# Kernel optimization log

Measured on AMD Instinct MI355X. Metric: run time of the kernel, lower is better.

Reference implementation:

```python
import jax, jax.numpy as jnp
import numpy as np


def _warp(x, flow):
    """Backward bilinear warp (grid_sample equivalent, zeros padding).

    x:    [B, C, H, W] feature frame
    flow: [B, 2, H, W] per-pixel motion vector (x, y) in pixels
    Samples x at (px + flow_x, py + flow_y) with bilinear interpolation;
    out-of-bounds samples contribute zero (padding_mode='zeros').
    """
    B, C, H, W = x.shape
    ys, xs = jnp.meshgrid(jnp.arange(H, dtype=x.dtype), jnp.arange(W, dtype=x.dtype), indexing='ij')
    gx = xs[None] + flow[:, 0]  # [B, H, W] sample x coords
    gy = ys[None] + flow[:, 1]  # [B, H, W] sample y coords
    x0 = jnp.floor(gx)
    y0 = jnp.floor(gy)
    wx = gx - x0
    wy = gy - y0
    flat = x.reshape(B, C, H * W)

    def corner(xi, yi, w):
        valid = (xi >= 0) & (xi <= W - 1) & (yi >= 0) & (yi <= H - 1)
        xc = jnp.clip(xi, 0, W - 1).astype(jnp.int32)
        yc = jnp.clip(yi, 0, H - 1).astype(jnp.int32)
        idx = (yc * W + xc).reshape(B, 1, H * W)
        v = jnp.take_along_axis(flat, idx, axis=2).reshape(B, C, H, W)
        return v * (w * valid.astype(x.dtype))[:, None]

    return (corner(x0, y0, (1.0 - wx) * (1.0 - wy))
            + corner(x0 + 1.0, y0, wx * (1.0 - wy))
            + corner(x0, y0 + 1.0, (1.0 - wx) * wy)
            + corner(x0 + 1.0, y0 + 1.0, wx * wy))


def setup_inputs() -> dict:
    key = jax.random.key(0)
    k1, k2 = jax.random.split(key)
    B, I, C, H, W = 2, 5, 16, 544, 960
    features = jax.random.normal(k1, (B, I, C, H, W), dtype=jnp.float32)
    mv = jax.random.normal(k2, (B, I, 2, H, W), dtype=jnp.float32) * 4.0  # ~4 px motion
    return {"features": features, "mv": mv}


def reference(features, mv):
    """Accumulative backward warp.

    Original torch loop: for i in 1..I-1: for j = i-1 .. 0:
        features[:, i] = warp(features[:, i], mv[:, j])
    i.e. frame i is sequentially warped by mv[i-1], mv[i-2], ..., mv[0].
    Equivalent vectorized form: for j = I-2 .. 0, warp all frames > j by
    mv[:, j] simultaneously (each frame still sees mv indices in descending
    order), removing the per-frame Python loop.
    """
    I = features.shape[1]
    warp_frames = jax.vmap(_warp, in_axes=(1, None), out_axes=1)  # over frame axis
    out = features
    for j in range(I - 2, -1, -1):
        warped = warp_frames(out[:, j + 1:], mv[:, j])  # [B, I-1-j, C, H, W]
        out = out.at[:, j + 1:].set(warped)
    return out
```

## Files before the change

### kernel.cpp

```cpp
#include <hip/hip_runtime.h>
#include <stdint.h>

namespace {
constexpr int Wd = 960, Hd = 544, Cd = 16, Id = 5, Bd = 2;
constexpr int HW = Hd * Wd;
constexpr long CHW = (long)Cd * HW;
constexpr long FRAME_BSTRIDE = (long)Id * CHW;
constexpr long FLOW_BSTRIDE  = (long)Id * 2 * HW;

constexpr int TSX = 64, TSY = 32;
constexpr int HALO = 12;
constexpr int TWX = TSX + 2 * HALO;
constexpr int TWY = TSY + 2 * HALO;
constexpr int NCHUNK = 20;
constexpr int TILE_F = NCHUNK * 256;
constexpr int GX = Wd / TSX;
constexpr int GY = Hd / TSY;
constexpr int NWG = GX * GY * Bd;
}

struct F2 { float x, y; };
struct Job {
  const void* s; long ss;
  void*       d; long ds;
  const float* fl;
  int sBF, dBF;
};

__device__ __forceinline__ uint f2bf_bits(float v) {
  uint x = __float_as_uint(v);
  return (x + 0x7FFFu + ((x >> 16) & 1u)) >> 16;
}

__global__ __launch_bounds__(512) void warp_jobs(
    Job j0, Job j1, Job j2, Job j3, Job j4)
{
  __shared__ float tile[2][TILE_F];

  const int jb = blockIdx.y;
  Job J = j0;
  if      (jb == 1) J = j1;
  else if (jb == 2) J = j2;
  else if (jb == 3) J = j3;
  else if (jb == 4) J = j4;

  const int orig = blockIdx.x;
  const int xcd  = orig & 7;
  constexpr int q = NWG / 8, r = NWG % 8;
  const int wgid = (xcd < r ? xcd * (q + 1) : r * (q + 1) + (xcd - r) * q)
                 + (orig >> 3);

  const int b   = wgid / (GX * GY);
  const int rem = wgid - b * (GX * GY);
  const int tyb = rem / GX;
  const int txb = rem - tyb * GX;
  const int X0 = txb * TSX;
  const int Y0 = tyb * TSY;

  const int t   = threadIdx.x;
  const int x   = X0 + ((t & 15) << 2);
  const int y   = Y0 + (t >> 4);
  const int pix = y * Wd + x;

  const float*    sF32 = (const float*)J.s + (long)b * J.ss;
  float*          dF32 = (float*)J.d + (long)b * J.ds;
  const uint16_t* sB16 = (const uint16_t*)J.s + (long)b * J.ss;
  uint16_t*       dB16 = (uint16_t*)J.d + (long)b * J.ds;
  const bool sBF = J.sBF != 0;
  const bool dBF = J.dBF != 0;

  if (J.fl == nullptr) {
#pragma unroll
    for (int c = 0; c < Cd; ++c)
      *reinterpret_cast<float4*>(dF32 + (long)c * HW + pix)
          = *reinterpret_cast<const float4*>(sF32 + (long)c * HW + pix);
    return;
  }

  const float* fl = J.fl + (long)b * FLOW_BSTRIDE;
  float4 fxv = *reinterpret_cast<const float4*>(fl + pix);
  float4 fyv = *reinterpret_cast<const float4*>(fl + HW + pix);

  float w00[4], w10[4], w01[4], w11[4];
  int   lA[4];
  int   g00[4], g10[4], g01[4], g11[4];

#pragma unroll
  for (int j = 0; j < 4; ++j) {
    float fx = (j == 0) ? fxv.x : (j == 1) ? fxv.y : (j == 2) ? fxv.z : fxv.w;
    float fy = (j == 0) ? fyv.x : (j == 1) ? fyv.y : (j == 2) ? fyv.z : fyv.w;
    float gx = (float)(x + j) + fx;
    float gy = (float)y + fy;
    float x0f = floorf(gx), y0f = floorf(gy);
    float wx = gx - x0f, wy = gy - y0f;
    bool vx0 = (x0f >= 0.f) && (x0f <= (float)(Wd - 1));
    bool vx1 = (x0f + 1.f >= 0.f) && (x0f + 1.f <= (float)(Wd - 1));
    bool vy0 = (y0f >= 0.f) && (y0f <= (float)(Hd - 1));
    bool vy1 = (y0f + 1.f >= 0.f) && (y0f + 1.f <= (float)(Hd - 1));
    w00[j] = (1.f - wx) * (1.f - wy) * ((vx0 && vy0) ? 1.f : 0.f);
    w10[j] = wx * (1.f - wy)         * ((vx1 && vy0) ? 1.f : 0.f);
    w01[j] = (1.f - wx) * wy         * ((vx0 && vy1) ? 1.f : 0.f);
    w11[j] = wx * wy                 * ((vx1 && vy1) ? 1.f : 0.f);
    int ix0 = (int)x0f;
    int iy0 = (int)y0f;
    int lx = ix0 - (X0 - HALO);
    int ly = iy0 - (Y0 - HALO);
    bool ft = (lx >= 0) & (lx <= TWX - 2) & (ly >= 0) & (ly <= TWY - 2);
    lA[j] = ft ? (ly * TWX + lx) * 4 : -1;
    int xc0 = min(max(ix0, 0), Wd - 1), xc1 = min(max(ix0 + 1, 0), Wd - 1);
    int yc0 = min(max(iy0, 0), Hd - 1), yc1 = min(max(iy0 + 1, 0), Hd - 1);
    g00[j] = yc0 * Wd + xc0;
    g10[j] = yc0 * Wd + xc1;
    g01[j] = yc1 * Wd + xc0;
    g11[j] = yc1 * Wd + xc1;
  }

  const int lane = t & 63;
  const int wv   = t >> 6;
  const int nck  = (wv < 4) ? 3 : 2;
  int goff[3];
#pragma unroll
  for (int k = 0; k < 3; ++k) {
    int ck = wv + 8 * k;
    if (ck < NCHUNK) {
      int foff = ck * 256 + lane * 4;
      int ly = foff / TWX;
      int lx = foff - ly * TWX;
      int gxc = min(max(X0 - HALO + lx, 0), Wd - 4);
      int gyc = min(max(Y0 - HALO + ly, 0), Hd - 1);
      goff[k] = gyc * Wd + gxc;
    }
  }

  auto fill32 = [&](int nb, int c) {
    const float* sC = sF32 + (long)c * HW;
#pragma unroll
    for (int k = 0; k < 3; ++k) {
      if (k < nck) {
        __builtin_amdgcn_global_load_lds(
            (__attribute__((address_space(1))) void*)(void*)(sC + goff[k]),
            (__attribute__((address_space(3))) void*)&tile[nb][(wv + 8 * k) * 256],
            16, 0, 0);
      }
    }
  };

  uint2 ld[3];
  auto loadB = [&](int c) {
    const uint* gp = (const uint*)(sB16 + (long)c * HW);
#pragma unroll
    for (int k = 0; k < 3; ++k)
      if (k < nck) ld[k] = *(const uint2*)(gp + (goff[k] >> 1));
  };
  auto writeB = [&](int nb) {
#pragma unroll
    for (int k = 0; k < 3; ++k) {
      if (k < nck) {
        float4 f;
        f.x = __uint_as_float(ld[k].x << 16);
        f.y = __uint_as_float(ld[k].x & 0xFFFF0000u);
        f.z = __uint_as_float(ld[k].y << 16);
        f.w = __uint_as_float(ld[k].y & 0xFFFF0000u);
        *reinterpret_cast<float4*>(&tile[nb][(wv + 8 * k) * 256 + lane * 4]) = f;
      }
    }
  };

  if (sBF) { loadB(0); writeB(0); } else fill32(0, 0);

#pragma unroll
  for (int c = 0; c < Cd; ++c) {
    __syncthreads();
    const bool pre = (c + 1 < Cd);
    if (pre) { if (sBF) loadB(c + 1); else fill32((c + 1) & 1, c + 1); }

    const float* tb = tile[c & 1];
    float ov[4];
#pragma unroll
    for (int j = 0; j < 4; ++j) {
      float v;
      if (lA[j] >= 0) {
        F2 r0 = *(const F2*)((const char*)tb + lA[j]);
        F2 r1 = *(const F2*)((const char*)tb + lA[j] + TWX * 4);
        v = (w00[j] * r0.x + w10[j] * r0.y) + (w01[j] * r1.x + w11[j] * r1.y);
      } else if (sBF) {
        const uint16_t* su = sB16 + (long)c * HW;
        float v00 = __uint_as_float((uint)su[g00[j]] << 16);
        float v10 = __uint_as_float((uint)su[g10[j]] << 16);
        float v01 = __uint_as_float((uint)su[g01[j]] << 16);
        float v11 = __uint_as_float((uint)su[g11[j]] << 16);
        v = w00[j] * v00 + w10[j] * v10 + w01[j] * v01 + w11[j] * v11;
      } else {
        const float* sC = sF32 + (long)c * HW;
        v = w00[j] * sC[g00[j]] + w10[j] * sC[g10[j]]
          + w01[j] * sC[g01[j]] + w11[j] * sC[g11[j]];
      }
      ov[j] = v;
    }
    if (dBF) {
      uint p0 = f2bf_bits(ov[0]) | (f2bf_bits(ov[1]) << 16);
      uint p1 = f2bf_bits(ov[2]) | (f2bf_bits(ov[3]) << 16);
      *reinterpret_cast<uint2*>(dB16 + (long)c * HW + pix) = make_uint2(p0, p1);
    } else {
      *reinterpret_cast<float4*>(dF32 + (long)c * HW + pix)
          = make_float4(ov[0], ov[1], ov[2], ov[3]);
    }
    if (pre && sBF) writeB((c + 1) & 1);
  }
}

extern "C" void kernel_launch(void* const* d_in, const int* in_sizes, int n_in,
                              void* d_out, int out_size, void* d_ws, size_t ws_size,
                              hipStream_t stream) {
  const float* feat = (const float*)d_in[0];
  const float* mv   = (const float*)d_in[1];
  float*       out  = (float*)d_out;

  dim3 block(512, 1, 1);
  const long FB = FRAME_BSTRIDE;
  auto mkjob = [](const void* s, long ss, void* d, long ds, const float* fl,
                  int sBF, int dBF) {
    Job j; j.s = s; j.ss = ss; j.d = d; j.ds = ds; j.fl = fl;
    j.sBF = sBF; j.dBF = dBF; return j;
  };
  Job Z = mkjob(nullptr, 0, nullptr, 0, nullptr, 0, 0);
  const float* flj[4] = { mv + 0L * 2 * HW, mv + 1L * 2 * HW,
                          mv + 2L * 2 * HW, mv + 3L * 2 * HW };

  auto launch = [&](int nj, Job a, Job b, Job c, Job d, Job e) {
    warp_jobs<<<dim3(NWG, nj, 1), block, 0, stream>>>(a, b, c, d, e);
  };

  const size_t need = (size_t)(4 * CHW) * Bd * sizeof(uint16_t);

  if (ws_size >= need) {
    uint16_t* W  = (uint16_t*)d_ws;
    const long WB = 4 * CHW;
    uint16_t* wa = W + 0 * CHW;
    uint16_t* wb = W + 1 * CHW;
    uint16_t* wd = W + 2 * CHW;
    uint16_t* wc = W + 3 * CHW;
    uint16_t* we = (uint16_t*)(out + 4 * CHW);
    const long EB = 2 * FB;

    launch(5,
      mkjob(feat + 1 * CHW, FB, out + 1 * CHW, FB, flj[0], 0, 0),
      mkjob(feat + 2 * CHW, FB, wa, WB, flj[1], 0, 1),
      mkjob(feat + 3 * CHW, FB, wb, WB, flj[2], 0, 1),
      mkjob(feat + 4 * CHW, FB, wd, WB, flj[3], 0, 1),
      mkjob(feat, FB, out, FB, nullptr, 0, 0));
    launch(3,
      mkjob(wa, WB, out + 2 * CHW, FB, flj[0], 1, 0),
      mkjob(wb, WB, wc, WB, flj[1], 1, 1),
      mkjob(wd, WB, we, EB, flj[2], 1, 1), Z, Z);
    launch(2,
      mkjob(wc, WB, out + 3 * CHW, FB, flj[0], 1, 0),
      mkjob(we, EB, wa, WB, flj[1], 1, 1), Z, Z, Z);
    launch(1, mkjob(wa, WB, out + 4 * CHW, FB, flj[0], 1, 0), Z, Z, Z, Z);
  } else {
    float* S = out;
    auto w1 = [&](const float* s, float* d, int j) {
      launch(1, mkjob(s, FB, d, FB, flj[j], 0, 0), Z, Z, Z, Z);
    };
    w1(feat + 1 * CHW, out + 1 * CHW, 0);
    w1(feat + 2 * CHW, S, 1);
    w1(S, out + 2 * CHW, 0);
    w1(feat + 3 * CHW, out + 3 * CHW, 2);
    w1(out + 3 * CHW, S, 1);
    w1(S, out + 3 * CHW, 0);
    w1(feat + 4 * CHW, S, 3);
    w1(S, out + 4 * CHW, 2);
    w1(out + 4 * CHW, S, 1);
    w1(S, out + 4 * CHW, 0);
    launch(1, mkjob(feat, FB, out, FB, nullptr, 0, 0), Z, Z, Z, Z);
  }
}
```

Baseline: 339.2 us.

## Split warp kernel into fp32 pipelined and bf16 variants with deferred fallback

```diff
diff --git a/kernel.cpp b/kernel.cpp
--- a/kernel.cpp
+++ b/kernel.cpp
@@ -20,22 +20,97 @@
 }
 
 struct F2 { float x, y; };
-struct Job {
-  const void* s; long ss;
-  void*       d; long ds;
-  const float* fl;
-  int sBF, dBF;
-};
+struct Job { const void* s; long ss; void* d; long ds; const float* fl; int sBF, dBF; };
 
 __device__ __forceinline__ uint f2bf_bits(float v) {
   uint x = __float_as_uint(v);
   return (x + 0x7FFFu + ((x >> 16) & 1u)) >> 16;
 }
 
-__global__ __launch_bounds__(512) void warp_jobs(
+#define DECODE_TILE()                                                        \
+  const int orig = blockIdx.x;                                               \
+  const int xcd  = orig & 7;                                                 \
+  constexpr int q = NWG / 8, r = NWG % 8;                                    \
+  const int wgid = (xcd < r ? xcd * (q + 1) : r * (q + 1) + (xcd - r) * q)   \
+                 + (orig >> 3);                                              \
+  const int b   = wgid / (GX * GY);                                          \
+  const int rem = wgid - b * (GX * GY);                                      \
+  const int tyb = rem / GX;                                                  \
+  const int txb = rem - tyb * GX;                                            \
+  const int X0 = txb * TSX;                                                  \
+  const int Y0 = tyb * TSY;                                                  \
+  const int t   = threadIdx.x;                                               \
+  const int x   = X0 + ((t & 15) << 2);                                      \
+  const int y   = Y0 + (t >> 4);                                             \
+  const int pix = y * Wd + x;
+
+#define PRECOMPUTE_WEIGHTS()                                                 \
+  float4 fxv = *reinterpret_cast<const float4*>(fl + pix);                   \
+  float4 fyv = *reinterpret_cast<const float4*>(fl + HW + pix);              \
+  float w00[4], w10[4], w01[4], w11[4];                                      \
+  int lA[4]; uint32_t pxy[4]; int fbm = 0;                                   \
+  _Pragma("unroll")                                                          \
+  for (int j = 0; j < 4; ++j) {                                              \
+    float fx = (j==0)?fxv.x:(j==1)?fxv.y:(j==2)?fxv.z:fxv.w;                 \
+    float fy = (j==0)?fyv.x:(j==1)?fyv.y:(j==2)?fyv.z:fyv.w;                 \
+    float gx = (float)(x + j) + fx;                                          \
+    float gy = (float)y + fy;                                                \
+    float x0f = floorf(gx), y0f = floorf(gy);                                \
+    float wx = gx - x0f, wy = gy - y0f;                                      \
+    bool vx0 = (x0f >= 0.f) && (x0f <= (float)(Wd - 1));                     \
+    bool vx1 = (x0f + 1.f >= 0.f) && (x0f + 1.f <= (float)(Wd - 1));         \
+    bool vy0 = (y0f >= 0.f) && (y0f <= (float)(Hd - 1));                     \
+    bool vy1 = (y0f + 1.f >= 0.f) && (y0f + 1.f <= (float)(Hd - 1));         \
+    w00[j] = (1.f-wx)*(1.f-wy) * ((vx0 && vy0) ? 1.f : 0.f);                 \
+    w10[j] = wx*(1.f-wy)       * ((vx1 && vy0) ? 1.f : 0.f);                 \
+    w01[j] = (1.f-wx)*wy       * ((vx0 && vy1) ? 1.f : 0.f);                 \
+    w11[j] = wx*wy             * ((vx1 && vy1) ? 1.f : 0.f);                 \
+    int ix0 = (int)x0f;                                                      \
+    int iy0 = (int)y0f;                                                      \
+    int lx = ix0 - (X0 - HALO);                                              \
+    int ly = iy0 - (Y0 - HALO);                                              \
+    bool ft = (lx >= 0) & (lx <= TWX - 2) & (ly >= 0) & (ly <= TWY - 2);     \
+    if (!ft) fbm |= (1 << j);                                                \
+    int lxc = min(max(lx, 0), TWX - 2), lyc = min(max(ly, 0), TWY - 2);      \
+    lA[j] = (lyc * TWX + lxc) * 4;                                           \
+    uint32_t px_ = (uint32_t)min(max(ix0 + 128, 0), 65535);                  \
+    uint32_t py_ = (uint32_t)min(max(iy0 + 128, 0), 65535);                  \
+    pxy[j] = px_ | (py_ << 16);                                              \
+  }
+
+#define PRECOMPUTE_GOFF()                                                    \
+  const int lane = t & 63;                                                   \
+  const int wv   = t >> 6;                                                   \
+  const int nck  = (wv < 4) ? 3 : 2;                                         \
+  int goff[3];                                                               \
+  _Pragma("unroll")                                                          \
+  for (int k = 0; k < 3; ++k) {                                              \
+    int ck = wv + 8 * k;                                                     \
+    if (ck < NCHUNK) {                                                       \
+      int foff = ck * 256 + lane * 4;                                        \
+      int ly = foff / TWX;                                                   \
+      int lx = foff - ly * TWX;                                              \
+      int gxc = min(max(X0 - HALO + lx, 0), Wd - 4);                         \
+      int gyc = min(max(Y0 - HALO + ly, 0), Hd - 1);                         \
+      goff[k] = gyc * Wd + gxc;                                              \
+    }                                                                        \
+  }
+
+#define WAITV(n3, n2)                                                        \
+  if (wv < 4) { asm volatile("s_waitcnt vmcnt(" #n3 ")" ::: "memory"); }     \
+  else        { asm volatile("s_waitcnt vmcnt(" #n2 ")" ::: "memory"); }
+
+#define PHASE(c, n3, n2)                                                     \
+  WAITV(n3, n2);                                                             \
+  __builtin_amdgcn_s_barrier();                                              \
+  __builtin_amdgcn_sched_barrier(0);                                         \
+  if ((c) + 3 < Cd) fillq(((c) + 3) & 3, (c) + 3);                           \
+  comp(c);
+
+__global__ __launch_bounds__(512, 4) void warp_pipe(
     Job j0, Job j1, Job j2, Job j3, Job j4)
 {
-  __shared__ float tile[2][TILE_F];
+  __shared__ float tile[4 * TILE_F];
 
   const int jb = blockIdx.y;
   Job J = j0;
@@ -44,29 +119,11 @@
   else if (jb == 3) J = j3;
   else if (jb == 4) J = j4;
 
-  const int orig = blockIdx.x;
-  const int xcd  = orig & 7;
-  constexpr int q = NWG / 8, r = NWG % 8;
-  const int wgid = (xcd < r ? xcd * (q + 1) : r * (q + 1) + (xcd - r) * q)
-                 + (orig >> 3);
-
-  const int b   = wgid / (GX * GY);
-  const int rem = wgid - b * (GX * GY);
-  const int tyb = rem / GX;
-  const int txb = rem - tyb * GX;
-  const int X0 = txb * TSX;
-  const int Y0 = tyb * TSY;
-
-  const int t   = threadIdx.x;
-  const int x   = X0 + ((t & 15) << 2);
-  const int y   = Y0 + (t >> 4);
-  const int pix = y * Wd + x;
-
-  const float*    sF32 = (const float*)J.s + (long)b * J.ss;
-  float*          dF32 = (float*)J.d + (long)b * J.ds;
-  const uint16_t* sB16 = (const uint16_t*)J.s + (long)b * J.ss;
-  uint16_t*       dB16 = (uint16_t*)J.d + (long)b * J.ds;
-  const bool sBF = J.sBF != 0;
+  DECODE_TILE();
+
+  const float* sF32 = (const float*)J.s + (long)b * J.ss;
+  float*       dF32 = (float*)J.d + (long)b * J.ds;
+  uint16_t*    dB16 = (uint16_t*)J.d + (long)b * J.ds;
   const bool dBF = J.dBF != 0;
 
   if (J.fl == nullptr) {
@@ -78,72 +135,95 @@
   }
 
   const float* fl = J.fl + (long)b * FLOW_BSTRIDE;
-  float4 fxv = *reinterpret_cast<const float4*>(fl + pix);
-  float4 fyv = *reinterpret_cast<const float4*>(fl + HW + pix);
-
-  float w00[4], w10[4], w01[4], w11[4];
-  int   lA[4];
-  int   g00[4], g10[4], g01[4], g11[4];
-
-#pragma unroll
-  for (int j = 0; j < 4; ++j) {
-    float fx = (j == 0) ? fxv.x : (j == 1) ? fxv.y : (j == 2) ? fxv.z : fxv.w;
-    float fy = (j == 0) ? fyv.x : (j == 1) ? fyv.y : (j == 2) ? fyv.z : fyv.w;
-    float gx = (float)(x + j) + fx;
-    float gy = (float)y + fy;
-    float x0f = floorf(gx), y0f = floorf(gy);
-    float wx = gx - x0f, wy = gy - y0f;
-    bool vx0 = (x0f >= 0.f) && (x0f <= (float)(Wd - 1));
-    bool vx1 = (x0f + 1.f >= 0.f) && (x0f + 1.f <= (float)(Wd - 1));
-    bool vy0 = (y0f >= 0.f) && (y0f <= (float)(Hd - 1));
-    bool vy1 = (y0f + 1.f >= 0.f) && (y0f + 1.f <= (float)(Hd - 1));
-    w00[j] = (1.f - wx) * (1.f - wy) * ((vx0 && vy0) ? 1.f : 0.f);
-    w10[j] = wx * (1.f - wy)         * ((vx1 && vy0) ? 1.f : 0.f);
-    w01[j] = (1.f - wx) * wy         * ((vx0 && vy1) ? 1.f : 0.f);
-    w11[j] = wx * wy                 * ((vx1 && vy1) ? 1.f : 0.f);
-    int ix0 = (int)x0f;
-    int iy0 = (int)y0f;
-    int lx = ix0 - (X0 - HALO);
-    int ly = iy0 - (Y0 - HALO);
-    bool ft = (lx >= 0) & (lx <= TWX - 2) & (ly >= 0) & (ly <= TWY - 2);
-    lA[j] = ft ? (ly * TWX + lx) * 4 : -1;
-    int xc0 = min(max(ix0, 0), Wd - 1), xc1 = min(max(ix0 + 1, 0), Wd - 1);
-    int yc0 = min(max(iy0, 0), Hd - 1), yc1 = min(max(iy0 + 1, 0), Hd - 1);
-    g00[j] = yc0 * Wd + xc0;
-    g10[j] = yc0 * Wd + xc1;
-    g01[j] = yc1 * Wd + xc0;
-    g11[j] = yc1 * Wd + xc1;
-  }
-
-  const int lane = t & 63;
-  const int wv   = t >> 6;
-  const int nck  = (wv < 4) ? 3 : 2;
-  int goff[3];
-#pragma unroll
-  for (int k = 0; k < 3; ++k) {
-    int ck = wv + 8 * k;
-    if (ck < NCHUNK) {
-      int foff = ck * 256 + lane * 4;
-      int ly = foff / TWX;
-      int lx = foff - ly * TWX;
-      int gxc = min(max(X0 - HALO + lx, 0), Wd - 4);
-      int gyc = min(max(Y0 - HALO + ly, 0), Hd - 1);
-      goff[k] = gyc * Wd + gxc;
-    }
-  }
-
-  auto fill32 = [&](int nb, int c) {
+  PRECOMPUTE_WEIGHTS();
+  PRECOMPUTE_GOFF();
+
+  auto fillq = [&](int buf, int c) {
     const float* sC = sF32 + (long)c * HW;
+    float* base = &tile[buf * TILE_F];
 #pragma unroll
     for (int k = 0; k < 3; ++k) {
       if (k < nck) {
         __builtin_amdgcn_global_load_lds(
             (__attribute__((address_space(1))) void*)(void*)(sC + goff[k]),
-            (__attribute__((address_space(3))) void*)&tile[nb][(wv + 8 * k) * 256],
+            (__attribute__((address_space(3))) void*)&base[(wv + 8 * k) * 256],
             16, 0, 0);
       }
     }
   };
+
+  auto comp = [&](int c) {
+    const float* tb = &tile[(c & 3) * TILE_F];
+    float ov[4];
+#pragma unroll
+    for (int j = 0; j < 4; ++j) {
+      F2 r0 = *(const F2*)((const char*)tb + lA[j]);
+      F2 r1 = *(const F2*)((const char*)tb + lA[j] + TWX * 4);
+      ov[j] = (w00[j] * r0.x + w10[j] * r0.y) + (w01[j] * r1.x + w11[j] * r1.y);
+    }
+    if (dBF) {
+      uint p0 = f2bf_bits(ov[0]) | (f2bf_bits(ov[1]) << 16);
+      uint p1 = f2bf_bits(ov[2]) | (f2bf_bits(ov[3]) << 16);
+      *reinterpret_cast<uint2*>(dB16 + (long)c * HW + pix) = make_uint2(p0, p1);
+    } else {
+      *reinterpret_cast<float4*>(dF32 + (long)c * HW + pix)
+          = make_float4(ov[0], ov[1], ov[2], ov[3]);
+    }
+  };
+
+  fillq(0, 0); fillq(1, 1); fillq(2, 2);
+
+  PHASE(0, 6, 4)  PHASE(1, 7, 5)  PHASE(2, 8, 6)
+  PHASE(3, 9, 7)  PHASE(4, 9, 7)  PHASE(5, 9, 7)
+  PHASE(6, 9, 7)  PHASE(7, 9, 7)  PHASE(8, 9, 7)
+  PHASE(9, 9, 7)  PHASE(10, 9, 7) PHASE(11, 9, 7)
+  PHASE(12, 9, 7) PHASE(13, 9, 7)
+  PHASE(14, 6, 5) PHASE(15, 3, 3)
+
+  if (fbm) {
+    asm volatile("s_waitcnt vmcnt(0)" ::: "memory");
+    for (int c = 0; c < Cd; ++c) {
+      const float* sC = sF32 + (long)c * HW;
+#pragma unroll
+      for (int j = 0; j < 4; ++j) {
+        if (fbm & (1 << j)) {
+          uint32_t p = pxy[j];
+          int ix0 = (int)(p & 0xffffu) - 128;
+          int iy0 = (int)(p >> 16) - 128;
+          int xc0 = min(max(ix0, 0), Wd - 1), xc1 = min(max(ix0 + 1, 0), Wd - 1);
+          int yc0 = min(max(iy0, 0), Hd - 1), yc1 = min(max(iy0 + 1, 0), Hd - 1);
+          float v = w00[j] * sC[yc0 * Wd + xc0] + w10[j] * sC[yc0 * Wd + xc1]
+                  + w01[j] * sC[yc1 * Wd + xc0] + w11[j] * sC[yc1 * Wd + xc1];
+          if (dBF) dB16[(long)c * HW + pix + j] = (uint16_t)f2bf_bits(v);
+          else     dF32[(long)c * HW + pix + j] = v;
+        }
+      }
+    }
+  }
+}
+
+__global__ __launch_bounds__(512) void warp_bf16(
+    Job j0, Job j1, Job j2, Job j3, Job j4)
+{
+  __shared__ float tile[2][TILE_F];
+
+  const int jb = blockIdx.y;
+  Job J = j0;
+  if      (jb == 1) J = j1;
+  else if (jb == 2) J = j2;
+  else if (jb == 3) J = j3;
+  else if (jb == 4) J = j4;
+
+  DECODE_TILE();
+
+  const uint16_t* sB16 = (const uint16_t*)J.s + (long)b * J.ss;
+  float*          dF32 = (float*)J.d + (long)b * J.ds;
+  uint16_t*       dB16 = (uint16_t*)J.d + (long)b * J.ds;
+  const bool dBF = J.dBF != 0;
+
+  const float* fl = J.fl + (long)b * FLOW_BSTRIDE;
+  PRECOMPUTE_WEIGHTS();
+  PRECOMPUTE_GOFF();
 
   uint2 ld[3];
   auto loadB = [&](int c) {
@@ -166,34 +246,35 @@
     }
   };
 
-  if (sBF) { loadB(0); writeB(0); } else fill32(0, 0);
+  loadB(0); writeB(0);
 
 #pragma unroll
   for (int c = 0; c < Cd; ++c) {
     __syncthreads();
     const bool pre = (c + 1 < Cd);
-    if (pre) { if (sBF) loadB(c + 1); else fill32((c + 1) & 1, c + 1); }
+    if (pre) loadB(c + 1);
 
     const float* tb = tile[c & 1];
     float ov[4];
 #pragma unroll
     for (int j = 0; j < 4; ++j) {
       float v;
-      if (lA[j] >= 0) {
+      if (!(fbm & (1 << j))) {
         F2 r0 = *(const F2*)((const char*)tb + lA[j]);
         F2 r1 = *(const F2*)((const char*)tb + lA[j] + TWX * 4);
         v = (w00[j] * r0.x + w10[j] * r0.y) + (w01[j] * r1.x + w11[j] * r1.y);
-      } else if (sBF) {
+      } else {
+        uint32_t p = pxy[j];
+        int ix0 = (int)(p & 0xffffu) - 128;
+        int iy0 = (int)(p >> 16) - 128;
+        int xc0 = min(max(ix0, 0), Wd - 1), xc1 = min(max(ix0 + 1, 0), Wd - 1);
+        int yc0 = min(max(iy0, 0), Hd - 1), yc1 = min(max(iy0 + 1, 0), Hd - 1);
         const uint16_t* su = sB16 + (long)c * HW;
-        float v00 = __uint_as_float((uint)su[g00[j]] << 16);
-        float v10 = __uint_as_float((uint)su[g10[j]] << 16);
-        float v01 = __uint_as_float((uint)su[g01[j]] << 16);
-        float v11 = __uint_as_float((uint)su[g11[j]] << 16);
+        float v00 = __uint_as_float((uint)su[yc0 * Wd + xc0] << 16);
+        float v10 = __uint_as_float((uint)su[yc0 * Wd + xc1] << 16);
+        float v01 = __uint_as_float((uint)su[yc1 * Wd + xc0] << 16);
+        float v11 = __uint_as_float((uint)su[yc1 * Wd + xc1] << 16);
         v = w00[j] * v00 + w10[j] * v10 + w01[j] * v01 + w11[j] * v11;
-      } else {
-        const float* sC = sF32 + (long)c * HW;
-        v = w00[j] * sC[g00[j]] + w10[j] * sC[g10[j]]
-          + w01[j] * sC[g01[j]] + w11[j] * sC[g11[j]];
       }
       ov[j] = v;
     }
@@ -205,7 +286,7 @@
       *reinterpret_cast<float4*>(dF32 + (long)c * HW + pix)
           = make_float4(ov[0], ov[1], ov[2], ov[3]);
     }
-    if (pre && sBF) writeB((c + 1) & 1);
+    if (pre) writeB((c + 1) & 1);
   }
 }
 
@@ -227,8 +308,11 @@
   const float* flj[4] = { mv + 0L * 2 * HW, mv + 1L * 2 * HW,
                           mv + 2L * 2 * HW, mv + 3L * 2 * HW };
 
-  auto launch = [&](int nj, Job a, Job b, Job c, Job d, Job e) {
-    warp_jobs<<<dim3(NWG, nj, 1), block, 0, stream>>>(a, b, c, d, e);
+  auto launchP = [&](int nj, Job a, Job b, Job c, Job d, Job e) {
+    warp_pipe<<<dim3(NWG, nj, 1), block, 0, stream>>>(a, b, c, d, e);
+  };
+  auto launchB = [&](int nj, Job a, Job b, Job c) {
+    warp_bf16<<<dim3(NWG, nj, 1), block, 0, stream>>>(a, b, c, Z, Z);
   };
 
   const size_t need = (size_t)(4 * CHW) * Bd * sizeof(uint16_t);
@@ -243,24 +327,24 @@
     uint16_t* we = (uint16_t*)(out + 4 * CHW);
     const long EB = 2 * FB;
 
-    launch(5,
+    launchP(5,
       mkjob(feat + 1 * CHW, FB, out + 1 * CHW, FB, flj[0], 0, 0),
       mkjob(feat + 2 * CHW, FB, wa, WB, flj[1], 0, 1),
       mkjob(feat + 3 * CHW, FB, wb, WB, flj[2], 0, 1),
       mkjob(feat + 4 * CHW, FB, wd, WB, flj[3], 0, 1),
       mkjob(feat, FB, out, FB, nullptr, 0, 0));
-    launch(3,
+    launchB(3,
       mkjob(wa, WB, out + 2 * CHW, FB, flj[0], 1, 0),
       mkjob(wb, WB, wc, WB, flj[1], 1, 1),
-      mkjob(wd, WB, we, EB, flj[2], 1, 1), Z, Z);
-    launch(2,
+      mkjob(wd, WB, we, EB, flj[2], 1, 1));
+    launchB(2,
       mkjob(wc, WB, out + 3 * CHW, FB, flj[0], 1, 0),
-      mkjob(we, EB, wa, WB, flj[1], 1, 1), Z, Z, Z);
-    launch(1, mkjob(wa, WB, out + 4 * CHW, FB, flj[0], 1, 0), Z, Z, Z, Z);
+      mkjob(we, EB, wa, WB, flj[1], 1, 1), Z);
+    launchB(1, mkjob(wa, WB, out + 4 * CHW, FB, flj[0], 1, 0), Z, Z);
   } else {
     float* S = out;
     auto w1 = [&](const float* s, float* d, int j) {
-      launch(1, mkjob(s, FB, d, FB, flj[j], 0, 0), Z, Z, Z, Z);
+      launchP(1, mkjob(s, FB, d, FB, flj[j], 0, 0), Z, Z, Z, Z);
     };
     w1(feat + 1 * CHW, out + 1 * CHW, 0);
     w1(feat + 2 * CHW, S, 1);
@@ -272,6 +356,6 @@
     w1(S, out + 4 * CHW, 2);
     w1(out + 4 * CHW, S, 1);
     w1(S, out + 4 * CHW, 0);
-    launch(1, mkjob(feat, FB, out, FB, nullptr, 0, 0), Z, Z, Z, Z);
-  }
-}
+    launchP(1, mkjob(feat, FB, out, FB, nullptr, 0, 0), Z, Z, Z, Z);
+  }
+}
```

After: 300.6 us. -11.4%, faster.
